# Optimization experiments

Measured on AMD Instinct MI355X. Metric: run time of the kernel, lower is better.

## Reference

```python
import jax, jax.numpy as jnp
import numpy as np

B, S, H = 2, 2048, 2048
NH = 16
HD = H // NH  # 128


def setup_inputs() -> dict:
    key = jax.random.key(0)
    ks = jax.random.split(key, 5)
    scale = 1.0 / np.sqrt(H)
    return {
        "hidden_states": jax.random.normal(ks[0], (B, S, H), dtype=jnp.float32),
        "attention_mask": jnp.zeros((B, 1, S, S), dtype=jnp.float32),
        "q_weight": jax.random.normal(ks[1], (H, H), dtype=jnp.float32) * scale,
        "k_weight": jax.random.normal(ks[2], (H, H), dtype=jnp.float32) * scale,
        "v_weight": jax.random.normal(ks[3], (H, H), dtype=jnp.float32) * scale,
        "o_weight": jax.random.normal(ks[4], (H, H), dtype=jnp.float32) * scale,
    }


def reference(hidden_states, attention_mask, q_weight, k_weight, v_weight, o_weight):
    b, s, h = hidden_states.shape
    # Linear(y = x @ W.T), then split heads: [b, nh, s, hd]
    q = (hidden_states @ q_weight.T).reshape(b, s, NH, HD).transpose(0, 2, 1, 3)
    k = (hidden_states @ k_weight.T).reshape(b, s, NH, HD).transpose(0, 2, 1, 3)
    v = (hidden_states @ v_weight.T).reshape(b, s, NH, HD).transpose(0, 2, 1, 3)
    scores = jnp.einsum("bhqd,bhkd->bhqk", q, k) / jnp.sqrt(jnp.float32(HD))
    scores = scores + attention_mask  # additive mask, broadcasts over heads
    attn = jax.nn.softmax(scores, axis=-1)
    out = jnp.einsum("bhqk,bhkd->bhqd", attn, v)
    out = out.transpose(0, 2, 1, 3).reshape(b, s, h)
    return out @ o_weight.T
```

## Files before the change

### kernel.cpp

```cpp
#include <hip/hip_runtime.h>
#include <stdint.h>

constexpr int SEQ   = 2048;
constexpr int NHEAD = 16;
constexpr int HDSZ  = 128;
constexpr int HDIM  = 2048;
constexpr float QK_SCALE = 0.08838834764831845f;

typedef __attribute__((ext_vector_type(8))) __bf16 bf16x8;
typedef __attribute__((ext_vector_type(4))) __bf16 bf16x4;
typedef __attribute__((ext_vector_type(2))) __bf16 bf16x2;
typedef __attribute__((ext_vector_type(4))) float  f32x4;

__device__ __forceinline__ void gl_lds16(const void* gptr, void* lptr) {
  __builtin_amdgcn_global_load_lds(
      (const __attribute__((address_space(1))) unsigned int*)gptr,
      (__attribute__((address_space(3))) unsigned int*)lptr, 16, 0, 0);
}

__global__ __launch_bounds__(256) void cast_f32_bf16(
    const float* __restrict__ in, __bf16* __restrict__ out, int n4) {
  int i = blockIdx.x * blockDim.x + threadIdx.x;
  int stride = gridDim.x * blockDim.x;
  for (; i < n4; i += stride) {
    float4 v = ((const float4*)in)[i];
    bf16x4 o = { (__bf16)v.x, (__bf16)v.y, (__bf16)v.z, (__bf16)v.w };
    ((bf16x4*)out)[i] = o;
  }
}

__global__ __launch_bounds__(256) void cast4_f32_bf16(
    const float* __restrict__ w0, const float* __restrict__ w1,
    const float* __restrict__ w2, const float* __restrict__ w3,
    __bf16* __restrict__ out, int n4) {
  const int y = blockIdx.y;
  const float* src = (y == 0) ? w0 : (y == 1) ? w1 : (y == 2) ? w2 : w3;
  __bf16* dst = out + (size_t)y * (size_t)n4 * 4;
  int i = blockIdx.x * blockDim.x + threadIdx.x;
  int stride = gridDim.x * blockDim.x;
  for (; i < n4; i += stride) {
    float4 v = ((const float4*)src)[i];
    bf16x4 o = { (__bf16)v.x, (__bf16)v.y, (__bf16)v.z, (__bf16)v.w };
    ((bf16x4*)dst)[i] = o;
  }
}

__global__ __launch_bounds__(256) void gemm_qkv(
    const __bf16* __restrict__ A, const __bf16* __restrict__ W,
    __bf16* __restrict__ qkv) {
  constexpr long XN = 4096L * 2048;
  constexpr int K = 2048;
  __shared__ __align__(16) char smem[2 * 16384];
  __bf16* Ts = (__bf16*)smem;

  const int tid  = threadIdx.x;
  const int lane = tid & 63;
  const int w    = tid >> 6;
  const int lg   = lane >> 4, lr = lane & 15;
  const int wr   = w >> 1, wc = w & 1;
  const int flat = blockIdx.y * 48 + blockIdx.x;
  const int swz  = (flat & 7) * 192 + (flat >> 3);
  const int mtile = swz & 31, ntile = swz >> 5;
  const long mbase = (long)mtile * 128;
  const long nbase = (long)ntile * 128;

  f32x4 acc[4][4];
#pragma unroll
  for (int i = 0; i < 4; ++i)
#pragma unroll
    for (int j = 0; j < 4; ++j) acc[i][j] = (f32x4){0.f, 0.f, 0.f, 0.f};

  const int srow = lane >> 2;
  const int scol = (lane & 3) * 8;

  auto stage = [&](int buf, int kt) {
    __bf16* As = (__bf16*)(smem + buf * 16384);
    __bf16* Bs = As + 128 * 32;
#pragma unroll
    for (int i = 0; i < 2; ++i) {
      const int c = w * 2 + i;
      gl_lds16(A + (mbase + c * 16 + srow) * (long)K + kt + scol, &As[c * 512]);
      gl_lds16(W + (nbase + c * 16 + srow) * (long)K + kt + scol, &Bs[c * 512]);
    }
  };

  stage(0, 0);
  __syncthreads();

  constexpr int NTK = K / 32;
  for (int t = 0; t < NTK; ++t) {
    const int cur = t & 1;
    if (t + 1 < NTK) stage(cur ^ 1, (t + 1) * 32);
    __builtin_amdgcn_sched_barrier(0);
    const __bf16* As = (const __bf16*)(smem + cur * 16384);
    const __bf16* Bs = As + 128 * 32;
    bf16x8 af[4], bfv[4];
#pragma unroll
    for (int mm = 0; mm < 4; ++mm)
      af[mm] = *(const bf16x8*)&As[(wr * 64 + mm * 16 + lr) * 32 + lg * 8];
#pragma unroll
    for (int nn = 0; nn < 4; ++nn)
      bfv[nn] = *(const bf16x8*)&Bs[(wc * 64 + nn * 16 + lr) * 32 + lg * 8];
    __builtin_amdgcn_s_setprio(1);
#pragma unroll
    for (int nn = 0; nn < 4; ++nn)
#pragma unroll
      for (int mm = 0; mm < 4; ++mm)
        acc[mm][nn] = __builtin_amdgcn_mfma_f32_16x16x32_bf16(
            af[mm], bfv[nn], acc[mm][nn], 0, 0, 0);
    __builtin_amdgcn_s_setprio(0);
    __syncthreads();
  }

  const int  mat = ntile >> 4;
  const long nb2 = nbase - (long)mat * 2048;
  const long b   = mbase >> 11, s0 = mbase & 2047;
  const long h   = nb2 >> 7;

  if (mat < 2) {
    __bf16* out = qkv + (size_t)mat * XN;
#pragma unroll
    for (int dh = 0; dh < 2; ++dh) {
      if (wr == dh) {
#pragma unroll
        for (int mm = 0; mm < 4; ++mm)
#pragma unroll
          for (int nn = 0; nn < 4; ++nn) {
            const int d = wc * 64 + nn * 16 + lr;
#pragma unroll
            for (int r = 0; r < 4; ++r)
              Ts[(mm * 16 + lg * 4 + r) * 136 + d] = (__bf16)acc[mm][nn][r];
          }
      }
      __syncthreads();
#pragma unroll
      for (int it = 0; it < 4; ++it) {
        const int idx = it * 256 + tid;
        const int row = idx >> 4, c = idx & 15;
        bf16x8 v = *(const bf16x8*)&Ts[row * 136 + c * 8];
        *(bf16x8*)&out[((b * NHEAD + h) * SEQ + s0 + dh * 64 + row) * HDSZ +
                       c * 8] = v;
      }
      __syncthreads();
    }
  } else {
    __bf16* out = qkv + 2 * XN;
#pragma unroll
    for (int dh = 0; dh < 2; ++dh) {
      if (wc == dh) {
#pragma unroll
        for (int mm = 0; mm < 4; ++mm)
#pragma unroll
          for (int nn = 0; nn < 4; ++nn) {
            const int dd = nn * 16 + lr;
            bf16x4 pk = { (__bf16)acc[mm][nn][0], (__bf16)acc[mm][nn][1],
                          (__bf16)acc[mm][nn][2], (__bf16)acc[mm][nn][3] };
            *(bf16x4*)&Ts[dd * 136 + wr * 64 + mm * 16 + lg * 4] = pk;
          }
      }
      __syncthreads();
#pragma unroll
      for (int it = 0; it < 4; ++it) {
        const int idx = it * 256 + tid;
        const int dd = idx >> 4, c = idx & 15;
        bf16x8 v = *(const bf16x8*)&Ts[dd * 136 + c * 8];
        *(bf16x8*)&out[((b * NHEAD + h) * HDSZ + dh * 64 + dd) * SEQ +
                       s0 + c * 8] = v;
      }
      __syncthreads();
    }
  }
}

__global__ __launch_bounds__(256) void gemm_bt_f32(
    const __bf16* __restrict__ A, const __bf16* __restrict__ B,
    float* __restrict__ C, int M, int N, int K) {
  __shared__ __align__(16) char smem[2 * 16384];
  const int tid  = threadIdx.x;
  const int lane = tid & 63;
  const int w    = tid >> 6;
  const int lg   = lane >> 4, lr = lane & 15;
  const int wr   = w >> 1, wc = w & 1;
  const int flat = blockIdx.y * 16 + blockIdx.x;
  const int swz  = (flat & 7) * 64 + (flat >> 3);
  const long mbase = (long)(swz >> 4) * 128;
  const long nbase = (long)(swz & 15) * 128;

  f32x4 acc[4][4];
#pragma unroll
  for (int i = 0; i < 4; ++i)
#pragma unroll
    for (int j = 0; j < 4; ++j) acc[i][j] = (f32x4){0.f, 0.f, 0.f, 0.f};

  const int srow = lane >> 2;
  const int scol = (lane & 3) * 8;

  auto stage = [&](int buf, int kt) {
    __bf16* As = (__bf16*)(smem + buf * 16384);
    __bf16* Bs = As + 128 * 32;
#pragma unroll
    for (int i = 0; i < 2; ++i) {
      const int c = w * 2 + i;
      gl_lds16(A + (mbase + c * 16 + srow) * (long)K + kt + scol, &As[c * 512]);
      gl_lds16(B + (nbase + c * 16 + srow) * (long)K + kt + scol, &Bs[c * 512]);
    }
  };

  stage(0, 0);
  __syncthreads();

  const int NTK = K / 32;
  for (int t = 0; t < NTK; ++t) {
    const int cur = t & 1;
    if (t + 1 < NTK) stage(cur ^ 1, (t + 1) * 32);
    __builtin_amdgcn_sched_barrier(0);
    const __bf16* As = (const __bf16*)(smem + cur * 16384);
    const __bf16* Bs = As + 128 * 32;
    bf16x8 af[4], bfv[4];
#pragma unroll
    for (int mm = 0; mm < 4; ++mm)
      af[mm] = *(const bf16x8*)&As[(wr * 64 + mm * 16 + lr) * 32 + lg * 8];
#pragma unroll
    for (int nn = 0; nn < 4; ++nn)
      bfv[nn] = *(const bf16x8*)&Bs[(wc * 64 + nn * 16 + lr) * 32 + lg * 8];
    __builtin_amdgcn_s_setprio(1);
#pragma unroll
    for (int nn = 0; nn < 4; ++nn)
#pragma unroll
      for (int mm = 0; mm < 4; ++mm)
        acc[mm][nn] = __builtin_amdgcn_mfma_f32_16x16x32_bf16(
            af[mm], bfv[nn], acc[mm][nn], 0, 0, 0);
    __builtin_amdgcn_s_setprio(0);
    __syncthreads();
  }

#pragma unroll
  for (int mm = 0; mm < 4; ++mm)
#pragma unroll
    for (int nn = 0; nn < 4; ++nn) {
      const long n = nbase + wc * 64 + nn * 16 + lr;
#pragma unroll
      for (int r = 0; r < 4; ++r) {
        const long m = mbase + wr * 64 + mm * 16 + lg * 4 + r;
        C[m * (long)N + n] = acc[mm][nn][r];
      }
    }
}

__global__ __launch_bounds__(512, 4) void attn_fused(
    const __bf16* __restrict__ Q, const __bf16* __restrict__ K,
    const __bf16* __restrict__ Vt, const float* __restrict__ mask,
    __bf16* __restrict__ Out) {
  __shared__ __bf16 Ks[2 * 64 * 128];
  __shared__ __bf16 Vs[2 * 128 * 64];
  __shared__ __bf16 Ps[128 * 64];

  const int tid  = threadIdx.x;
  const int lane = tid & 63;
  const int w    = tid >> 6;
  const int lg   = lane >> 4, lr = lane & 15;
  const int flat = blockIdx.y * 16 + blockIdx.x;
  const int swz  = (flat & 7) * 64 + (flat >> 3);
  const int bh   = swz >> 4;
  const int b    = bh >> 4, h = bh & 15;
  const int q0   = (swz & 15) * 128;

  const __bf16* Qh = Q  + (size_t)bh * SEQ * HDSZ;
  const __bf16* Kh = K  + (size_t)bh * SEQ * HDSZ;
  const __bf16* Vh = Vt + (size_t)bh * HDSZ * SEQ;
  const float*  Mb = mask + (size_t)b * SEQ * SEQ;

  bf16x8 qf[4];
#pragma unroll
  for (int kk = 0; kk < 4; ++kk)
    qf[kk] = *(const bf16x8*)(
        Qh + (size_t)(q0 + w * 16 + lr) * HDSZ + kk * 32 + lg * 8);

  const __bf16* ksrc[2];
  const __bf16* vsrc[2];
#pragma unroll
  for (int i = 0; i < 2; ++i) {
    const int ch = i * 512 + tid;
    const int krow = ch >> 4, kc = ch & 15;
    ksrc[i] = Kh + (size_t)krow * HDSZ + (((kc & 8) | ((kc ^ krow) & 7)) * 8);
    const int vrow = ch >> 3, vc = ch & 7;
    vsrc[i] = Vh + (size_t)vrow * SEQ + (((vc ^ vrow) & 7) * 8);
  }

  float mrw = -1e30f, lrw = 0.f;
  f32x4 acco[8];
#pragma unroll
  for (int n = 0; n < 8; ++n) acco[n] = (f32x4){0.f, 0.f, 0.f, 0.f};

#pragma unroll
  for (int i = 0; i < 2; ++i) {
    gl_lds16(ksrc[i], &Ks[(i * 512 + w * 64) * 8]);
    gl_lds16(vsrc[i], &Vs[(i * 512 + w * 64) * 8]);
  }
  __syncthreads();

  constexpr int NT = SEQ / 64;
  for (int t = 0; t < NT; ++t) {
    const int cur = t & 1;
    const int kt = t * 64;
    const char* Kb = (const char*)(Ks + cur * (64 * 128));
    const char* Vb = (const char*)(Vs + cur * (128 * 64));

    f32x4 mk[4];
#pragma unroll
    for (int n = 0; n < 4; ++n)
      mk[n] = *(const f32x4*)(
          Mb + (size_t)(q0 + w * 16 + lr) * SEQ + kt + n * 16 + lg * 4);
    __builtin_amdgcn_sched_barrier(0);

    if (t + 1 < NT) {
      const int nk = kt + 64;
      __bf16* Kn = Ks + (cur ^ 1) * (64 * 128);
      __bf16* Vn = Vs + (cur ^ 1) * (128 * 64);
#pragma unroll
      for (int i = 0; i < 2; ++i) {
        gl_lds16(ksrc[i] + (size_t)nk * HDSZ, &Kn[(i * 512 + w * 64) * 8]);
        gl_lds16(vsrc[i] + nk, &Vn[(i * 512 + w * 64) * 8]);
      }
    }
    __builtin_amdgcn_sched_barrier(0);

    f32x4 sacc[4];
#pragma unroll
    for (int n = 0; n < 4; ++n) sacc[n] = (f32x4){0.f, 0.f, 0.f, 0.f};
    __builtin_amdgcn_s_setprio(1);
#pragma unroll
    for (int n = 0; n < 4; ++n)
#pragma unroll
      for (int kk = 0; kk < 4; ++kk) {
        const int cp = (kk * 4 + lg) ^ (lr & 7);
        bf16x8 kf = *(const bf16x8*)(Kb + ((n * 16 + lr) << 8) + (cp << 4));
        sacc[n] = __builtin_amdgcn_mfma_f32_16x16x32_bf16(kf, qf[kk], sacc[n], 0, 0, 0);
      }
    __builtin_amdgcn_s_setprio(0);

    float sv[4][4];
    float tm = -1e30f;
#pragma unroll
    for (int n = 0; n < 4; ++n)
#pragma unroll
      for (int r = 0; r < 4; ++r) {
        float x = fmaf(sacc[n][r], QK_SCALE, mk[n][r]);
        sv[n][r] = x;
        tm = fmaxf(tm, x);
      }
    tm = fmaxf(tm, __shfl_xor(tm, 16));
    tm = fmaxf(tm, __shfl_xor(tm, 32));
    const float mn = fmaxf(mrw, tm);
    const float corr = __expf(mrw - mn);
    mrw = mn;
    float ls = 0.f;
#pragma unroll
    for (int n = 0; n < 4; ++n)
#pragma unroll
      for (int r = 0; r < 4; ++r) {
        float p = __expf(sv[n][r] - mn);
        sv[n][r] = p;
        ls += p;
      }
    ls += __shfl_xor(ls, 16);
    ls += __shfl_xor(ls, 32);
    lrw = lrw * corr + ls;
    float cb[4];
#pragma unroll
    for (int r = 0; r < 4; ++r) cb[r] = __shfl(corr, lg * 4 + r);
#pragma unroll
    for (int n = 0; n < 8; ++n)
#pragma unroll
      for (int r = 0; r < 4; ++r) acco[n][r] *= cb[r];

#pragma unroll
    for (int n = 0; n < 4; ++n)
#pragma unroll
      for (int rp = 0; rp < 2; ++rp) {
        bf16x2 pk = { (__bf16)sv[n][2 * rp], (__bf16)sv[n][2 * rp + 1] };
        const int pbyte = (n * 32 + lg * 8 + rp * 4) ^ ((lr & 7) << 4);
        *(bf16x2*)((char*)Ps + (w * 16 + lr) * 128 + pbyte) = pk;
      }
    __asm__ volatile("s_waitcnt lgkmcnt(0)" ::: "memory");
    __builtin_amdgcn_sched_barrier(0);

    __builtin_amdgcn_s_setprio(1);
#pragma unroll
    for (int kk = 0; kk < 2; ++kk) {
      const int pcp = (kk * 4 + lg) ^ (lr & 7);
      bf16x8 pa = *(const bf16x8*)(
          (const char*)Ps + (w * 16 + lr) * 128 + (pcp << 4));
#pragma unroll
      for (int n = 0; n < 8; ++n) {
        const int cp = (kk * 4 + lg) ^ (lr & 7);
        bf16x8 vf = *(const bf16x8*)(Vb + ((n * 16 + lr) << 7) + (cp << 4));
        acco[n] = __builtin_amdgcn_mfma_f32_16x16x32_bf16(pa, vf, acco[n], 0, 0, 0);
      }
    }
    __builtin_amdgcn_s_setprio(0);

    __syncthreads();
  }

  float lb[4];
#pragma unroll
  for (int r = 0; r < 4; ++r) lb[r] = __shfl(lrw, lg * 4 + r);
#pragma unroll
  for (int r = 0; r < 4; ++r) {
    const float inv = 1.0f / lb[r];
    const int srow = q0 + w * 16 + lg * 4 + r;
    const size_t base = ((size_t)b * SEQ + srow) * HDIM + h * HDSZ;
#pragma unroll
    for (int n = 0; n < 8; ++n)
      Out[base + n * 16 + lr] = (__bf16)(acco[n][r] * inv);
  }
}

extern "C" void kernel_launch(void* const* d_in, const int* in_sizes, int n_in,
                              void* d_out, int out_size, void* d_ws, size_t ws_size,
                              hipStream_t stream) {
  const float* x    = (const float*)d_in[0];
  const float* mask = (const float*)d_in[1];
  const float* wq   = (const float*)d_in[2];
  const float* wk   = (const float*)d_in[3];
  const float* wv   = (const float*)d_in[4];
  const float* wo   = (const float*)d_in[5];

  constexpr long XN = 4096L * 2048;
  constexpr long WN = 2048L * 2048;

  __bf16* xbf = (__bf16*)d_ws;
  __bf16* wqb = xbf + XN;
  __bf16* wob = wqb + 3 * WN;
  __bf16* qw  = wqb + 4 * WN;
  __bf16* kw  = qw + XN;
  __bf16* vtw = kw + XN;
  __bf16* aw  = vtw + XN;

  cast_f32_bf16<<<2048, 256, 0, stream>>>(x, xbf, (int)(XN / 4));
  cast4_f32_bf16<<<dim3(256, 4), 256, 0, stream>>>(wq, wk, wv, wo, wqb,
                                                   (int)(WN / 4));

  gemm_qkv<<<dim3(48, 32), 256, 0, stream>>>(xbf, wqb, qw);

  attn_fused<<<dim3(16, 32), 512, 0, stream>>>(qw, kw, vtw, mask, aw);

  gemm_bt_f32<<<dim3(16, 32), 256, 0, stream>>>(aw, wob, (float*)d_out,
                                                4096, 2048, 2048);
}
```

Baseline: 326.4 us.

## Process two query row-tiles per warp in attention and peel GEMM loop tail

Each attention block now covers 256 query rows instead of 128. Each warp handles two 16-row tiles, so every K and V fragment read from LDS feeds two MFMAs, and the grid is halved. This is meant to cut the LDS reads and the K/V global-to-LDS traffic per unit of work. In exchange it raises register pressure, lowers the occupancy hint to 2, and gives only 256 blocks. Both GEMMs also precompute their source pointers and peel the last k-iteration to drop the per-iteration branch.

```diff
diff --git a/kernel.cpp b/kernel.cpp
--- a/kernel.cpp
+++ b/kernel.cpp
@@ -73,26 +73,27 @@
   const int srow = lane >> 2;
   const int scol = (lane & 3) * 8;
 
+  const __bf16* asrc[2];
+  const __bf16* wsrc[2];
+#pragma unroll
+  for (int i = 0; i < 2; ++i) {
+    const int c = w * 2 + i;
+    asrc[i] = A + (mbase + c * 16 + srow) * (long)K + scol;
+    wsrc[i] = W + (nbase + c * 16 + srow) * (long)K + scol;
+  }
+
   auto stage = [&](int buf, int kt) {
     __bf16* As = (__bf16*)(smem + buf * 16384);
     __bf16* Bs = As + 128 * 32;
 #pragma unroll
     for (int i = 0; i < 2; ++i) {
       const int c = w * 2 + i;
-      gl_lds16(A + (mbase + c * 16 + srow) * (long)K + kt + scol, &As[c * 512]);
-      gl_lds16(W + (nbase + c * 16 + srow) * (long)K + kt + scol, &Bs[c * 512]);
+      gl_lds16(asrc[i] + kt, &As[c * 512]);
+      gl_lds16(wsrc[i] + kt, &Bs[c * 512]);
     }
   };
-
-  stage(0, 0);
-  __syncthreads();
-
-  constexpr int NTK = K / 32;
-  for (int t = 0; t < NTK; ++t) {
-    const int cur = t & 1;
-    if (t + 1 < NTK) stage(cur ^ 1, (t + 1) * 32);
-    __builtin_amdgcn_sched_barrier(0);
-    const __bf16* As = (const __bf16*)(smem + cur * 16384);
+  auto compute = [&](int buf) {
+    const __bf16* As = (const __bf16*)(smem + buf * 16384);
     const __bf16* Bs = As + 128 * 32;
     bf16x8 af[4], bfv[4];
 #pragma unroll
@@ -109,8 +110,20 @@
         acc[mm][nn] = __builtin_amdgcn_mfma_f32_16x16x32_bf16(
             af[mm], bfv[nn], acc[mm][nn], 0, 0, 0);
     __builtin_amdgcn_s_setprio(0);
+  };
+
+  stage(0, 0);
+  __syncthreads();
+
+  constexpr int NTK = K / 32;
+  for (int t = 0; t < NTK - 1; ++t) {
+    stage((t & 1) ^ 1, (t + 1) * 32);
+    __builtin_amdgcn_sched_barrier(0);
+    compute(t & 1);
     __syncthreads();
   }
+  compute((NTK - 1) & 1);
+  __syncthreads();
 
   const int  mat = ntile >> 4;
   const long nb2 = nbase - (long)mat * 2048;
@@ -195,26 +208,27 @@
   const int srow = lane >> 2;
   const int scol = (lane & 3) * 8;
 
+  const __bf16* asrc[2];
+  const __bf16* bsrc[2];
+#pragma unroll
+  for (int i = 0; i < 2; ++i) {
+    const int c = w * 2 + i;
+    asrc[i] = A + (mbase + c * 16 + srow) * (long)K + scol;
+    bsrc[i] = B + (nbase + c * 16 + srow) * (long)K + scol;
+  }
+
   auto stage = [&](int buf, int kt) {
     __bf16* As = (__bf16*)(smem + buf * 16384);
     __bf16* Bs = As + 128 * 32;
 #pragma unroll
     for (int i = 0; i < 2; ++i) {
       const int c = w * 2 + i;
-      gl_lds16(A + (mbase + c * 16 + srow) * (long)K + kt + scol, &As[c * 512]);
-      gl_lds16(B + (nbase + c * 16 + srow) * (long)K + kt + scol, &Bs[c * 512]);
+      gl_lds16(asrc[i] + kt, &As[c * 512]);
+      gl_lds16(bsrc[i] + kt, &Bs[c * 512]);
     }
   };
-
-  stage(0, 0);
-  __syncthreads();
-
-  const int NTK = K / 32;
-  for (int t = 0; t < NTK; ++t) {
-    const int cur = t & 1;
-    if (t + 1 < NTK) stage(cur ^ 1, (t + 1) * 32);
-    __builtin_amdgcn_sched_barrier(0);
-    const __bf16* As = (const __bf16*)(smem + cur * 16384);
+  auto compute = [&](int buf) {
+    const __bf16* As = (const __bf16*)(smem + buf * 16384);
     const __bf16* Bs = As + 128 * 32;
     bf16x8 af[4], bfv[4];
 #pragma unroll
@@ -231,8 +245,19 @@
         acc[mm][nn] = __builtin_amdgcn_mfma_f32_16x16x32_bf16(
             af[mm], bfv[nn], acc[mm][nn], 0, 0, 0);
     __builtin_amdgcn_s_setprio(0);
+  };
+
+  stage(0, 0);
+  __syncthreads();
+
+  const int NTK = K / 32;
+  for (int t = 0; t < NTK - 1; ++t) {
+    stage((t & 1) ^ 1, (t + 1) * 32);
+    __builtin_amdgcn_sched_barrier(0);
+    compute(t & 1);
     __syncthreads();
   }
+  compute((NTK - 1) & 1);
 
 #pragma unroll
   for (int mm = 0; mm < 4; ++mm)
@@ -247,34 +272,36 @@
     }
 }
 
-__global__ __launch_bounds__(512, 4) void attn_fused(
+__global__ __launch_bounds__(512, 2) void attn_fused(
     const __bf16* __restrict__ Q, const __bf16* __restrict__ K,
     const __bf16* __restrict__ Vt, const float* __restrict__ mask,
     __bf16* __restrict__ Out) {
   __shared__ __bf16 Ks[2 * 64 * 128];
   __shared__ __bf16 Vs[2 * 128 * 64];
-  __shared__ __bf16 Ps[128 * 64];
+  __shared__ __bf16 Ps[256 * 64];
 
   const int tid  = threadIdx.x;
   const int lane = tid & 63;
   const int w    = tid >> 6;
   const int lg   = lane >> 4, lr = lane & 15;
-  const int flat = blockIdx.y * 16 + blockIdx.x;
-  const int swz  = (flat & 7) * 64 + (flat >> 3);
-  const int bh   = swz >> 4;
+  const int flat = blockIdx.y * 8 + blockIdx.x;
+  const int swz  = (flat & 7) * 32 + (flat >> 3);
+  const int bh   = swz >> 3;
   const int b    = bh >> 4, h = bh & 15;
-  const int q0   = (swz & 15) * 128;
+  const int q0   = (swz & 7) * 256;
 
   const __bf16* Qh = Q  + (size_t)bh * SEQ * HDSZ;
   const __bf16* Kh = K  + (size_t)bh * SEQ * HDSZ;
   const __bf16* Vh = Vt + (size_t)bh * HDSZ * SEQ;
   const float*  Mb = mask + (size_t)b * SEQ * SEQ;
 
-  bf16x8 qf[4];
-#pragma unroll
-  for (int kk = 0; kk < 4; ++kk)
-    qf[kk] = *(const bf16x8*)(
-        Qh + (size_t)(q0 + w * 16 + lr) * HDSZ + kk * 32 + lg * 8);
+  bf16x8 qf[2][4];
+#pragma unroll
+  for (int rt = 0; rt < 2; ++rt)
+#pragma unroll
+    for (int kk = 0; kk < 4; ++kk)
+      qf[rt][kk] = *(const bf16x8*)(
+          Qh + (size_t)(q0 + w * 32 + rt * 16 + lr) * HDSZ + kk * 32 + lg * 8);
 
   const __bf16* ksrc[2];
   const __bf16* vsrc[2];
@@ -287,10 +314,12 @@
     vsrc[i] = Vh + (size_t)vrow * SEQ + (((vc ^ vrow) & 7) * 8);
   }
 
-  float mrw = -1e30f, lrw = 0.f;
-  f32x4 acco[8];
-#pragma unroll
-  for (int n = 0; n < 8; ++n) acco[n] = (f32x4){0.f, 0.f, 0.f, 0.f};
+  float mrw[2] = {-1e30f, -1e30f}, lrw[2] = {0.f, 0.f};
+  f32x4 acco[2][8];
+#pragma unroll
+  for (int rt = 0; rt < 2; ++rt)
+#pragma unroll
+    for (int n = 0; n < 8; ++n) acco[rt][n] = (f32x4){0.f, 0.f, 0.f, 0.f};
 
 #pragma unroll
   for (int i = 0; i < 2; ++i) {
@@ -306,11 +335,14 @@
     const char* Kb = (const char*)(Ks + cur * (64 * 128));
     const char* Vb = (const char*)(Vs + cur * (128 * 64));
 
-    f32x4 mk[4];
-#pragma unroll
-    for (int n = 0; n < 4; ++n)
-      mk[n] = *(const f32x4*)(
-          Mb + (size_t)(q0 + w * 16 + lr) * SEQ + kt + n * 16 + lg * 4);
+    f32x4 mk[2][4];
+#pragma unroll
+    for (int rt = 0; rt < 2; ++rt)
+#pragma unroll
+      for (int n = 0; n < 4; ++n)
+        mk[rt][n] = *(const f32x4*)(
+            Mb + (size_t)(q0 + w * 32 + rt * 16 + lr) * SEQ + kt +
+            n * 16 + lg * 4);
     __builtin_amdgcn_sched_barrier(0);
 
     if (t + 1 < NT) {
@@ -325,9 +357,11 @@
     }
     __builtin_amdgcn_sched_barrier(0);
 
-    f32x4 sacc[4];
-#pragma unroll
-    for (int n = 0; n < 4; ++n) sacc[n] = (f32x4){0.f, 0.f, 0.f, 0.f};
+    f32x4 sacc[2][4];
+#pragma unroll
+    for (int rt = 0; rt < 2; ++rt)
+#pragma unroll
+      for (int n = 0; n < 4; ++n) sacc[rt][n] = (f32x4){0.f, 0.f, 0.f, 0.f};
     __builtin_amdgcn_s_setprio(1);
 #pragma unroll
     for (int n = 0; n < 4; ++n)
@@ -335,53 +369,56 @@
       for (int kk = 0; kk < 4; ++kk) {
         const int cp = (kk * 4 + lg) ^ (lr & 7);
         bf16x8 kf = *(const bf16x8*)(Kb + ((n * 16 + lr) << 8) + (cp << 4));
-        sacc[n] = __builtin_amdgcn_mfma_f32_16x16x32_bf16(kf, qf[kk], sacc[n], 0, 0, 0);
+        sacc[0][n] = __builtin_amdgcn_mfma_f32_16x16x32_bf16(kf, qf[0][kk], sacc[0][n], 0, 0, 0);
+        sacc[1][n] = __builtin_amdgcn_mfma_f32_16x16x32_bf16(kf, qf[1][kk], sacc[1][n], 0, 0, 0);
       }
     __builtin_amdgcn_s_setprio(0);
 
-    float sv[4][4];
-    float tm = -1e30f;
-#pragma unroll
-    for (int n = 0; n < 4; ++n)
-#pragma unroll
-      for (int r = 0; r < 4; ++r) {
-        float x = fmaf(sacc[n][r], QK_SCALE, mk[n][r]);
-        sv[n][r] = x;
-        tm = fmaxf(tm, x);
-      }
-    tm = fmaxf(tm, __shfl_xor(tm, 16));
-    tm = fmaxf(tm, __shfl_xor(tm, 32));
-    const float mn = fmaxf(mrw, tm);
-    const float corr = __expf(mrw - mn);
-    mrw = mn;
-    float ls = 0.f;
-#pragma unroll
-    for (int n = 0; n < 4; ++n)
-#pragma unroll
-      for (int r = 0; r < 4; ++r) {
-        float p = __expf(sv[n][r] - mn);
-        sv[n][r] = p;
-        ls += p;
-      }
-    ls += __shfl_xor(ls, 16);
-    ls += __shfl_xor(ls, 32);
-    lrw = lrw * corr + ls;
-    float cb[4];
-#pragma unroll
-    for (int r = 0; r < 4; ++r) cb[r] = __shfl(corr, lg * 4 + r);
-#pragma unroll
-    for (int n = 0; n < 8; ++n)
-#pragma unroll
-      for (int r = 0; r < 4; ++r) acco[n][r] *= cb[r];
-
-#pragma unroll
-    for (int n = 0; n < 4; ++n)
-#pragma unroll
-      for (int rp = 0; rp < 2; ++rp) {
-        bf16x2 pk = { (__bf16)sv[n][2 * rp], (__bf16)sv[n][2 * rp + 1] };
-        const int pbyte = (n * 32 + lg * 8 + rp * 4) ^ ((lr & 7) << 4);
-        *(bf16x2*)((char*)Ps + (w * 16 + lr) * 128 + pbyte) = pk;
-      }
+#pragma unroll
+    for (int rt = 0; rt < 2; ++rt) {
+      float sv[4][4];
+      float tm = -1e30f;
+#pragma unroll
+      for (int n = 0; n < 4; ++n)
+#pragma unroll
+        for (int r = 0; r < 4; ++r) {
+          float x = fmaf(sacc[rt][n][r], QK_SCALE, mk[rt][n][r]);
+          sv[n][r] = x;
+          tm = fmaxf(tm, x);
+        }
+      tm = fmaxf(tm, __shfl_xor(tm, 16));
+      tm = fmaxf(tm, __shfl_xor(tm, 32));
+      const float mn = fmaxf(mrw[rt], tm);
+      const float corr = __expf(mrw[rt] - mn);
+      mrw[rt] = mn;
+      float ls = 0.f;
+#pragma unroll
+      for (int n = 0; n < 4; ++n)
+#pragma unroll
+        for (int r = 0; r < 4; ++r) {
+          float p = __expf(sv[n][r] - mn);
+          sv[n][r] = p;
+          ls += p;
+        }
+      ls += __shfl_xor(ls, 16);
+      ls += __shfl_xor(ls, 32);
+      lrw[rt] = lrw[rt] * corr + ls;
+      float cb[4];
+#pragma unroll
+      for (int r = 0; r < 4; ++r) cb[r] = __shfl(corr, lg * 4 + r);
+#pragma unroll
+      for (int n = 0; n < 8; ++n)
+#pragma unroll
+        for (int r = 0; r < 4; ++r) acco[rt][n][r] *= cb[r];
+#pragma unroll
+      for (int n = 0; n < 4; ++n)
+#pragma unroll
+        for (int rp = 0; rp < 2; ++rp) {
+          bf16x2 pk = { (__bf16)sv[n][2 * rp], (__bf16)sv[n][2 * rp + 1] };
+          const int pbyte = (n * 32 + lg * 8 + rp * 4) ^ ((lr & 7) << 4);
+          *(bf16x2*)((char*)Ps + (w * 32 + rt * 16 + lr) * 128 + pbyte) = pk;
+        }
+    }
     __asm__ volatile("s_waitcnt lgkmcnt(0)" ::: "memory");
     __builtin_amdgcn_sched_barrier(0);
 
@@ -389,13 +426,16 @@
 #pragma unroll
     for (int kk = 0; kk < 2; ++kk) {
       const int pcp = (kk * 4 + lg) ^ (lr & 7);
-      bf16x8 pa = *(const bf16x8*)(
-          (const char*)Ps + (w * 16 + lr) * 128 + (pcp << 4));
+      bf16x8 pa0 = *(const bf16x8*)(
+          (const char*)Ps + (w * 32 + lr) * 128 + (pcp << 4));
+      bf16x8 pa1 = *(const bf16x8*)(
+          (const char*)Ps + (w * 32 + 16 + lr) * 128 + (pcp << 4));
 #pragma unroll
       for (int n = 0; n < 8; ++n) {
         const int cp = (kk * 4 + lg) ^ (lr & 7);
         bf16x8 vf = *(const bf16x8*)(Vb + ((n * 16 + lr) << 7) + (cp << 4));
-        acco[n] = __builtin_amdgcn_mfma_f32_16x16x32_bf16(pa, vf, acco[n], 0, 0, 0);
+        acco[0][n] = __builtin_amdgcn_mfma_f32_16x16x32_bf16(pa0, vf, acco[0][n], 0, 0, 0);
+        acco[1][n] = __builtin_amdgcn_mfma_f32_16x16x32_bf16(pa1, vf, acco[1][n], 0, 0, 0);
       }
     }
     __builtin_amdgcn_s_setprio(0);
@@ -403,17 +443,20 @@
     __syncthreads();
   }
 
-  float lb[4];
-#pragma unroll
-  for (int r = 0; r < 4; ++r) lb[r] = __shfl(lrw, lg * 4 + r);
-#pragma unroll
-  for (int r = 0; r < 4; ++r) {
-    const float inv = 1.0f / lb[r];
-    const int srow = q0 + w * 16 + lg * 4 + r;
-    const size_t base = ((size_t)b * SEQ + srow) * HDIM + h * HDSZ;
-#pragma unroll
-    for (int n = 0; n < 8; ++n)
-      Out[base + n * 16 + lr] = (__bf16)(acco[n][r] * inv);
+#pragma unroll
+  for (int rt = 0; rt < 2; ++rt) {
+    float lb[4];
+#pragma unroll
+    for (int r = 0; r < 4; ++r) lb[r] = __shfl(lrw[rt], lg * 4 + r);
+#pragma unroll
+    for (int r = 0; r < 4; ++r) {
+      const float inv = 1.0f / lb[r];
+      const int srow = q0 + w * 32 + rt * 16 + lg * 4 + r;
+      const size_t base = ((size_t)b * SEQ + srow) * HDIM + h * HDSZ;
+#pragma unroll
+      for (int n = 0; n < 8; ++n)
+        Out[base + n * 16 + lr] = (__bf16)(acco[rt][n][r] * inv);
+    }
   }
 }
 
@@ -444,7 +487,7 @@
 
   gemm_qkv<<<dim3(48, 32), 256, 0, stream>>>(xbf, wqb, qw);
 
-  attn_fused<<<dim3(16, 32), 512, 0, stream>>>(qw, kw, vtw, mask, aw);
+  attn_fused<<<dim3(8, 32), 512, 0, stream>>>(qw, kw, vtw, mask, aw);
 
   gemm_bt_f32<<<dim3(16, 32), 256, 0, stream>>>(aw, wob, (float*)d_out,
                                                 4096, 2048, 2048);
```

Result: slower. 338.4 us (+3.7%).
